# Kernel tuning notes

Measured on AMD Instinct MI355X. Metric: run time of the kernel, lower is better.

Reference implementation:

```python
import jax, jax.numpy as jnp
import numpy as np

B, S, D = 8, 1024, 512
H, DH, OUT = 8, 64, 512
EPS = 1e-6

def _ln(x, scale, bias):
    m = jnp.mean(x, -1, keepdims=True)
    v = jnp.mean(jnp.square(x - m), -1, keepdims=True)
    return (x - m) * jax.lax.rsqrt(v + EPS) * scale + bias

def _rel_shift(x):
    # TransformerXL relative shift: [B,H,Q,P] -> [B,H,Q,P]
    b, h, q, p = x.shape
    x = jnp.pad(x, ((0, 0), (0, 0), (0, 0), (1, 0)))
    x = x.reshape(b, h, p + 1, q)
    return x[:, :, 1:, :].reshape(b, h, q, p)

def _gate(x, y, wry, wrx, wzy, wzx, why, whx, bg):
    # GTrXL GRU-style gating
    r = jax.nn.sigmoid(y @ wry + x @ wrx)
    z = jax.nn.sigmoid(y @ wzy + x @ wzx - bg)
    h = jnp.tanh(y @ why + (r * x) @ whx)
    return (1 - z) * x + z * h

def setup_inputs() -> dict:
    key = jax.random.key(0)
    ks = jax.random.split(key, 40)
    w = lambda k, shp: (0.02 * jax.random.normal(k, shp, jnp.float32))
    inp = {
        'values_keys': jax.random.normal(ks[0], (B, S, D), jnp.float32),
        'queries': jax.random.normal(ks[1], (B, S, D), jnp.float32),
        'pos_embed': jax.random.normal(ks[2], (S, D), jnp.float32),
        'mask': jnp.tril(jnp.ones((S, S), bool))[None, None],
        'ln1_scale': jnp.ones((D,), jnp.float32), 'ln1_bias': jnp.zeros((D,), jnp.float32),
        'wq': w(ks[3], (D, H, DH)), 'bq': jnp.zeros((H, DH), jnp.float32),
        'wk': w(ks[4], (D, H, DH)), 'bk': jnp.zeros((H, DH), jnp.float32),
        'wv': w(ks[5], (D, H, DH)), 'bv': jnp.zeros((H, DH), jnp.float32),
        'wr': w(ks[6], (D, H, DH)),
        'u_bias': w(ks[7], (H, DH)), 'v_bias': w(ks[8], (H, DH)),
        'wo': w(ks[9], (H, DH, OUT)), 'bo': jnp.zeros((OUT,), jnp.float32),
        'ln2_scale': jnp.ones((OUT,), jnp.float32), 'ln2_bias': jnp.zeros((OUT,), jnp.float32),
        'w1': w(ks[10], (OUT, OUT)), 'b1': jnp.zeros((OUT,), jnp.float32),
        'w2': w(ks[11], (OUT, OUT)), 'b2': jnp.zeros((OUT,), jnp.float32),
    }
    for gi, base in ((1, 12), (2, 19)):
        for j, nm in enumerate(['wry', 'wrx', 'wzy', 'wzx', 'why', 'whx']):
            inp['g%d_%s' % (gi, nm)] = w(ks[base + j], (OUT, OUT))
        inp['g%d_bg' % gi] = 2.0 * jnp.ones((OUT,), jnp.float32)
    return inp

def reference(values_keys, queries, pos_embed, mask, ln1_scale, ln1_bias, wq, bq, wk, bk, wv, bv, wr, u_bias, v_bias, wo, bo, ln2_scale, ln2_bias, w1, b1, w2, b2, g1_wry, g1_wrx, g1_wzy, g1_wzx, g1_why, g1_whx, g1_bg, g2_wry, g2_wrx, g2_wzy, g2_wzx, g2_why, g2_whx, g2_bg):
    vk = _ln(values_keys, ln1_scale, ln1_bias)
    qn = _ln(queries, ln1_scale, ln1_bias)
    q = jnp.einsum('bsd,dhk->bshk', qn, wq) + bq
    k = jnp.einsum('bsd,dhk->bshk', vk, wk) + bk
    v = jnp.einsum('bsd,dhk->bshk', vk, wv) + bv
    r = jnp.einsum('pd,dhk->phk', pos_embed, wr)
    ac = jnp.einsum('bqhk,bshk->bhqs', q + u_bias, k)
    bd = _rel_shift(jnp.einsum('bqhk,phk->bhqp', q + v_bias, r))
    scores = (ac + bd) * jnp.float32(1.0 / np.sqrt(DH))
    scores = jnp.where(mask, scores, jnp.float32(-1e9))
    attn = jax.nn.softmax(scores, axis=-1)
    o = jnp.einsum('bhqs,bshk->bqhk', attn, v)
    attn_out = jnp.einsum('bqhk,hko->bqo', o, wo) + bo
    out_attention = _gate(queries, jax.nn.relu(attn_out), g1_wry, g1_wrx, g1_wzy, g1_wzx, g1_why, g1_whx, g1_bg)
    h = _ln(out_attention, ln2_scale, ln2_bias)
    h = jax.nn.gelu(h @ w1 + b1) @ w2 + b2
    return _gate(h, jax.nn.relu(out_attention), g2_wry, g2_wrx, g2_wzy, g2_wzx, g2_why, g2_whx, g2_bg)
```

## Files before the change

kernel.cpp:

```cpp
#include <hip/hip_runtime.h>
#include <hip/hip_bf16.h>
#include <math.h>

#define TPB 256
#define B_   8
#define S_   1024
#define D_   512
#define H_   8
#define DH_  64
#define MTOK (B_ * S_)
#define NEL  (MTOK * D_)
#define WMAT (D_ * D_)

typedef __attribute__((ext_vector_type(8))) short bf8;
typedef __attribute__((ext_vector_type(4))) float f4;

__device__ __forceinline__ float ld_any(const void* p, long i, bool bf) {
  if (bf) {
    unsigned u = (unsigned)((const unsigned short*)p)[i];
    union { unsigned u; float f; } c; c.u = u << 16;
    return c.f;
  }
  return ((const float*)p)[i];
}

__device__ __forceinline__ unsigned short f2bf(float f) {
  union { float f; unsigned u; } c; c.f = f;
  unsigned u = c.u;
  u += 0x7FFFu + ((u >> 16) & 1u);
  return (unsigned short)(u >> 16);
}

typedef const void __attribute__((address_space(1)))* gp_t;
typedef void __attribute__((address_space(3)))* lp_t;
__device__ __forceinline__ void gl16(const void* g, void* l) {
  __builtin_amdgcn_global_load_lds((gp_t)(uintptr_t)g,
                                   (lp_t)(unsigned)(uintptr_t)l, 16, 0, 0);
}

struct P19 { const void* p[19]; };
struct P14 { const void* p[14]; };

__device__ __forceinline__ void ln_row_wave(
    const void* src, unsigned short* dst, long row,
    const void* scale, const void* bias, bool bf_s, bool bf_p, int lane,
    float* __restrict__ qF, unsigned short* __restrict__ qB) {
  const long base = row * 512 + lane * 8;
  float x[8];
  if (bf_s) {
    bf8 v = *(const bf8*)((const unsigned short*)src + base);
#pragma unroll
    for (int j = 0; j < 8; j++) {
      union { unsigned u; float f; } c;
      c.u = ((unsigned)(unsigned short)v[j]) << 16;
      x[j] = c.f;
    }
  } else {
    f4 a = *(const f4*)((const float*)src + base);
    f4 b = *(const f4*)((const float*)src + base + 4);
#pragma unroll
    for (int j = 0; j < 4; j++) { x[j] = a[j]; x[4 + j] = b[j]; }
  }
  if (qF) {
    f4 a, b;
#pragma unroll
    for (int j = 0; j < 4; j++) { a[j] = x[j]; b[j] = x[4 + j]; }
    *(f4*)(qF + base) = a;
    *(f4*)(qF + base + 4) = b;
    union { bf8 v; unsigned short s[8]; } q;
#pragma unroll
    for (int j = 0; j < 8; j++) q.s[j] = f2bf(x[j]);
    *(bf8*)(qB + base) = q.v;
  }
  float s = 0.f;
#pragma unroll
  for (int j = 0; j < 8; j++) s += x[j];
#pragma unroll
  for (int o = 1; o < 64; o <<= 1) s += __shfl_xor(s, o, 64);
  const float m = s * (1.0f / 512.0f);
  float vs = 0.f;
#pragma unroll
  for (int j = 0; j < 8; j++) { float d = x[j] - m; vs += d * d; }
#pragma unroll
  for (int o = 1; o < 64; o <<= 1) vs += __shfl_xor(vs, o, 64);
  const float inv = rsqrtf(vs * (1.0f / 512.0f) + 1e-6f);
  float sc[8], bi[8];
  if (bf_p) {
    bf8 vs_ = *(const bf8*)((const unsigned short*)scale + lane * 8);
    bf8 vb  = *(const bf8*)((const unsigned short*)bias + lane * 8);
#pragma unroll
    for (int j = 0; j < 8; j++) {
      union { unsigned u; float f; } c1, c2;
      c1.u = ((unsigned)(unsigned short)vs_[j]) << 16;
      c2.u = ((unsigned)(unsigned short)vb[j]) << 16;
      sc[j] = c1.f; bi[j] = c2.f;
    }
  } else {
    f4 s0 = *(const f4*)((const float*)scale + lane * 8);
    f4 s1 = *(const f4*)((const float*)scale + lane * 8 + 4);
    f4 b0 = *(const f4*)((const float*)bias + lane * 8);
    f4 b1 = *(const f4*)((const float*)bias + lane * 8 + 4);
#pragma unroll
    for (int j = 0; j < 4; j++) { sc[j] = s0[j]; sc[4 + j] = s1[j];
                                  bi[j] = b0[j]; bi[4 + j] = b1[j]; }
  }
  union { bf8 v; unsigned short s8[8]; } o;
#pragma unroll
  for (int j = 0; j < 8; j++) o.s8[j] = f2bf((x[j] - m) * inv * sc[j] + bi[j]);
  *(bf8*)(dst + base) = o.v;
}

__global__ __launch_bounds__(TPB) void k_prep(
    const void* __restrict__ vk_src, const void* __restrict__ q_src,
    const void* __restrict__ pos_src, const void* __restrict__ sc_src,
    const void* __restrict__ bi_src, P19 pw, P14 pp,
    unsigned short* __restrict__ vk_b, unsigned short* __restrict__ qn_b,
    float* __restrict__ qF, unsigned short* __restrict__ qB,
    unsigned short* __restrict__ posB, float* __restrict__ Pb,
    unsigned short* __restrict__ Wt, const unsigned* __restrict__ flagp) {
  __shared__ float smem[64 * 65];
  const bool bf = (*flagp == 0x3F803F80u);
  const int bx = blockIdx.x, t = threadIdx.x;
  const int lane = t & 63, w = t >> 6;
  if (bx < 4096) {
    long row = (long)bx * 4 + w;
    if (row < MTOK) {
      ln_row_wave(vk_src, vk_b, row, sc_src, bi_src, bf, bf, lane,
                  nullptr, nullptr);
    } else {
      ln_row_wave(q_src, qn_b, row - MTOK, sc_src, bi_src, bf, bf, lane,
                  qF, qB);
    }
  } else if (bx < 4608) {
    long i0 = ((long)(bx - 4096) * TPB + t) * 4;
#pragma unroll
    for (int j = 0; j < 4; j++) posB[i0 + j] = f2bf(ld_any(pos_src, i0 + j, bf));
  } else if (bx < 4636) {
    int i = (bx - 4608) * TPB + t;
    Pb[i] = ld_any(pp.p[i >> 9], i & 511, bf);
  } else {
    int zz = bx - 4636;
    int z = zz >> 6, tile = zz & 63;
    int k0 = (tile >> 3) * 64, n0 = (tile & 7) * 64;
    const void* src = pw.p[z];
    unsigned short* dst = Wt + (size_t)z * WMAT;
#pragma unroll
    for (int i = 0; i < 16; i++) {
      int fl = i * TPB + t;
      int r = fl >> 6, c = fl & 63;
      smem[r * 65 + c] = ld_any(src, (long)(k0 + r) * 512 + n0 + c, bf);
    }
    __syncthreads();
#pragma unroll
    for (int i = 0; i < 16; i++) {
      int fl = i * TPB + t;
      int r = fl >> 6, c = fl & 63;
      dst[(size_t)(n0 + r) * 512 + k0 + c] = f2bf(smem[c * 65 + r]);
    }
  }
}

__global__ __launch_bounds__(TPB) void k_ln_bf(const void* __restrict__ src,
                                               unsigned short* __restrict__ dst,
                                               const float* __restrict__ scale,
                                               const float* __restrict__ bias) {
  const int lane = threadIdx.x & 63, w = threadIdx.x >> 6;
  ln_row_wave(src, dst, (long)blockIdx.x * 4 + w, scale, bias, false, false,
              lane, nullptr, nullptr);
}

__global__ __launch_bounds__(TPB) void k_frag(
    const unsigned short* __restrict__ kB, const unsigned short* __restrict__ vTB,
    const unsigned short* __restrict__ rB, unsigned short* __restrict__ KF,
    unsigned short* __restrict__ VF, unsigned short* __restrict__ RF) {
  int c = blockIdx.x * TPB + threadIdx.x;
  if (c < 524288) {
    int col = c & 15, quad = (c >> 4) & 3, ks = (c >> 6) & 1, h = (c >> 7) & 7;
    int pg = (c >> 10) & 63, b = c >> 16;
    bf8 v = *(const bf8*)&kB[(size_t)(b * 1024 + pg * 16 + col) * 512 +
                             h * 64 + ks * 32 + quad * 8];
    *(bf8*)&KF[(size_t)c * 8] = v;
  } else if (c < 1048576) {
    int d = c - 524288;
    int col = d & 15, quad = (d >> 4) & 3, nd = (d >> 6) & 3, ks = (d >> 8) & 1;
    int pt = (d >> 9) & 15, h = (d >> 13) & 7, b = d >> 16;
    bf8 v = *(const bf8*)&vTB[(size_t)((b * 8 + h) * 64 + nd * 16 + col) * 1024 +
                              pt * 64 + ks * 32 + quad * 8];
    *(bf8*)&VF[(size_t)d * 8] = v;
  } else {
    int d = c - 1048576;
    int col = d & 15, quad = (d >> 4) & 3, ks = (d >> 6) & 1, g = (d >> 7) & 63;
    int h = d >> 13;
    bf8 v = *(const bf8*)&rB[(size_t)(g * 16 + col) * 512 +
                             h * 64 + ks * 32 + quad * 8];
    *(bf8*)&RF[(size_t)d * 8] = v;
  }
}

template <int ACT, bool DUAL>
__device__ __forceinline__ void gemm_core(
    unsigned short* As, unsigned short* Bs,
    const unsigned short* __restrict__ A1, const unsigned short* __restrict__ W1,
    const unsigned short* __restrict__ A2, const unsigned short* __restrict__ W2,
    const float* __restrict__ bias, const float* __restrict__ xb,
    const float* __restrict__ zb, const float* __restrict__ aux1,
    const float* __restrict__ aux2,
    float* __restrict__ outF, unsigned short* __restrict__ outB,
    unsigned short* __restrict__ outB2,
    const unsigned* __restrict__ flagp, int bm, int bn) {
  const int tid = threadIdx.x;
  const int w = tid >> 6, lane = tid & 63;
  const int quad = lane >> 4, col = lane & 15;
  const int wm = w >> 1, wn = w & 1;
  const int lrow = lane >> 3;
  const int lkc  = (lane & 7) ^ lrow;
  const int sw_base = col & 7;

  f4 acc[4][4];
#pragma unroll
  for (int mi = 0; mi < 4; mi++)
#pragma unroll
    for (int ni = 0; ni < 4; ni++) acc[mi][ni] = (f4){0.f, 0.f, 0.f, 0.f};

  auto stage = [&](const unsigned short* Ap, const unsigned short* Wp, int k0) {
#pragma unroll
    for (int i = 0; i < 4; i++) {
      gl16(Ap + (size_t)(bm + w * 32 + i * 8 + lrow) * 512 + k0 + lkc * 8,
           (char*)As + w * 4096 + i * 1024);
      gl16(Wp + (size_t)(bn + w * 32 + i * 8 + lrow) * 512 + k0 + lkc * 8,
           (char*)Bs + w * 4096 + i * 1024);
    }
  };
  auto compute = [&]() {
#pragma unroll
    for (int kk = 0; kk < 2; ++kk) {
      const int swz = (kk * 4 + quad) ^ sw_base;
      bf8 af[4], bfg[4];
#pragma unroll
      for (int mi = 0; mi < 4; mi++)
        af[mi] = *(const bf8*)&As[((wm * 64 + mi * 16 + col) * 8 + swz) * 8];
#pragma unroll
      for (int ni = 0; ni < 4; ni++)
        bfg[ni] = *(const bf8*)&Bs[((wn * 64 + ni * 16 + col) * 8 + swz) * 8];
#pragma unroll
      for (int mi = 0; mi < 4; mi++)
#pragma unroll
        for (int ni = 0; ni < 4; ni++)
          acc[mi][ni] = __builtin_amdgcn_mfma_f32_16x16x32_bf16(af[mi], bfg[ni],
                                                                acc[mi][ni], 0, 0, 0);
    }
  };

  for (int k0 = 0; k0 < 512; k0 += 64) {
    __syncthreads();
    stage(A1, W1, k0);
    __syncthreads();
    compute();
  }
  if constexpr (DUAL) {
    for (int k0 = 0; k0 < 512; k0 += 64) {
      __syncthreads();
      stage(A2, W2, k0);
      __syncthreads();
      compute();
    }
  }

  bool bfout = false;
  if constexpr (ACT == 7) bfout = (*flagp == 0x3F803F80u);
#pragma unroll
  for (int mi = 0; mi < 4; mi++)
#pragma unroll
    for (int ni = 0; ni < 4; ni++) {
      const int n = bn + wn * 64 + ni * 16 + col;
      const float bn_v = bias ? bias[n] : 0.f;
      const int m0 = bm + wm * 64 + mi * 16 + quad * 4;
      if (ACT == 11 && n >= 512) {
        unsigned long long pk = 0;
#pragma unroll
        for (int r = 0; r < 4; r++) {
          float v = acc[mi][ni][r] + bn_v;
          pk |= (unsigned long long)f2bf(v) << (16 * r);
        }
        size_t dst = ((size_t)(m0 >> 10) * 512 + (n - 512)) * 1024 + (m0 & 1023);
        *(unsigned long long*)&outB2[dst] = pk;
      } else {
#pragma unroll
        for (int r = 0; r < 4; r++) {
          size_t idx = (size_t)(m0 + r) * 512 + n;
          float v = acc[mi][ni][r] + bn_v;
          if (ACT == 0) {
            if (outF) outF[idx] = v;
            if (outB) outB[idx] = f2bf(v);
          } else if (ACT == 1) {
            outB[idx] = f2bf(fmaxf(v, 0.f));
          } else if (ACT == 5) {
            float z = zb[idx], x = xb[idx];
            float g = (1.f - z) * x + z * tanhf(v);
            outF[idx] = g;
            outB[idx] = f2bf(fmaxf(g, 0.f));
          } else if (ACT == 6) {
            float t = 0.7978845608028654f * (v + 0.044715f * v * v * v);
            outB[idx] = f2bf(0.5f * v * (1.f + tanhf(t)));
          } else if (ACT == 7) {
            float z = zb[idx], x = xb[idx];
            float g = (1.f - z) * x + z * tanhf(v);
            if (bfout) outB[idx] = f2bf(g);
            else       outF[idx] = g;
          } else if (ACT == 8) {
            outB[idx]  = f2bf(v + aux1[n]);
            outB2[idx] = f2bf(v + aux2[n]);
          } else if (ACT == 10) {
            if (n < 512) {
              outB[idx] = f2bf(xb[idx] / (1.f + __expf(-v)));
            } else {
              size_t zi = (size_t)(m0 + r) * 512 + (n - 512);
              outF[zi] = 1.f / (1.f + __expf(-(v - aux1[n - 512])));
            }
          } else if (ACT == 11) {
            outB[idx] = f2bf(v);
          }
        }
      }
    }
}

template <int ACT, bool DUAL>
__global__ __launch_bounds__(TPB) void k_gemm(
    const unsigned short* __restrict__ A1, const unsigned short* __restrict__ W1,
    const unsigned short* __restrict__ A2, const unsigned short* __restrict__ W2,
    const float* __restrict__ bias, const float* __restrict__ xb,
    const float* __restrict__ zb, const float* __restrict__ aux1,
    const float* __restrict__ aux2,
    float* __restrict__ outF, unsigned short* __restrict__ outB,
    unsigned short* __restrict__ outB2,
    const unsigned* __restrict__ flagp) {
  __shared__ unsigned short As[128 * 64];
  __shared__ unsigned short Bs[128 * 64];
  gemm_core<ACT, DUAL>(As, Bs, A1, W1, A2, W2, bias, xb, zb, aux1, aux2,
                       outF, outB, outB2, flagp,
                       blockIdx.x * 128, blockIdx.y * 128);
}

__global__ __launch_bounds__(TPB) void k_proj(
    const unsigned short* __restrict__ qn_b, const unsigned short* __restrict__ vk_b,
    const unsigned short* __restrict__ pos_b, const unsigned short* __restrict__ Wt,
    const float* __restrict__ Pb,
    unsigned short* __restrict__ qu_b, unsigned short* __restrict__ qv_b,
    unsigned short* __restrict__ k_b, unsigned short* __restrict__ vT,
    unsigned short* __restrict__ r_b) {
  __shared__ unsigned short As[128 * 64];
  __shared__ unsigned short Bs[128 * 64];
  const int bx = blockIdx.x;
  if (bx < 256) {
    int bm = (bx & 63) * 128, bn = (bx >> 6) * 128;
    gemm_core<8, false>(As, Bs, qn_b, Wt, nullptr, nullptr, Pb + 1024, nullptr,
                        nullptr, Pb + 2560, Pb + 3072, nullptr, qu_b, qv_b,
                        nullptr, bm, bn);
  } else if (bx < 768) {
    int t = bx - 256;
    int bm = (t & 63) * 128, bn = (t >> 6) * 128;
    gemm_core<11, false>(As, Bs, vk_b, Wt + (size_t)1 * WMAT, nullptr, nullptr,
                         Pb + 1536, nullptr, nullptr, nullptr, nullptr, nullptr,
                         k_b, vT, nullptr, bm, bn);
  } else {
    int t = bx - 768;
    int bm = (t & 7) * 128, bn = (t >> 3) * 128;
    gemm_core<0, false>(As, Bs, pos_b, Wt + (size_t)3 * WMAT, nullptr, nullptr,
                        nullptr, nullptr, nullptr, nullptr, nullptr, nullptr,
                        r_b, nullptr, nullptr, bm, bn);
  }
}

#define AC_STR 68
#define BD_STR 68

__global__ __launch_bounds__(64, 2) void k_attn8(
    const unsigned short* __restrict__ quB, const unsigned short* __restrict__ qvB,
    const unsigned short* __restrict__ KF, const unsigned short* __restrict__ VF,
    const unsigned short* __restrict__ RF, unsigned short* __restrict__ oB) {
  __shared__ float acS[16 * AC_STR];
  __shared__ float bdS[16 * BD_STR];
  const int lane = threadIdx.x;
  const int quad = lane >> 4, col = lane & 15;
  const int bx = blockIdx.x;
  const int bh = (bx & 7) * 8 + ((bx >> 3) & 7);
  const int qt = 63 - (bx >> 6);
  const int b = bh >> 3, h = bh & 7, dbase = h * 64;
  const int q0 = qt << 4;
  const int np = (qt >> 2) + 1;

  bf8 aqu[2], aqv[2];
  {
    const unsigned short* p1 = quB + (size_t)(b * 1024 + q0 + col) * 512 + dbase + quad * 8;
    const unsigned short* p2 = qvB + (size_t)(b * 1024 + q0 + col) * 512 + dbase + quad * 8;
    aqu[0] = *(const bf8*)p1; aqu[1] = *(const bf8*)(p1 + 32);
    aqv[0] = *(const bf8*)p2; aqv[1] = *(const bf8*)(p2 + 32);
  }
  f4 accO[4];
#pragma unroll
  for (int nd = 0; nd < 4; nd++) accO[nd] = (f4){0.f, 0.f, 0.f, 0.f};
  float lsum = 0.f;

  bf8 kreg[2][4], rreg[2][5], vreg[2][4];

  auto loadKR = [&](int pt) {
    const int pg = pt * 4;
    const int g0 = 63 - qt + pt * 4;
#pragma unroll
    for (int ks = 0; ks < 2; ++ks) {
#pragma unroll
      for (int ni = 0; ni < 4; ++ni) {
        size_t kidx = ((((size_t)b * 64 + pg + ni) * 8 + h) * 2 + ks) * 64 + lane;
        kreg[ks][ni] = *(const bf8*)&KF[kidx * 8];
      }
#pragma unroll
      for (int nj = 0; nj < 5; ++nj) {
        int g = g0 + nj; if (g > 63) g = 63;
        size_t ridx = (((size_t)h * 64 + g) * 2 + ks) * 64 + lane;
        rreg[ks][nj] = *(const bf8*)&RF[ridx * 8];
      }
    }
  };
  auto loadV = [&](int pt) {
#pragma unroll
    for (int ks = 0; ks < 2; ++ks)
#pragma unroll
      for (int nd = 0; nd < 4; ++nd) {
        size_t vidx = (((((size_t)b * 8 + h) * 16 + pt) * 2 + ks) * 4 + nd) * 64 + lane;
        vreg[ks][nd] = *(const bf8*)&VF[vidx * 8];
      }
  };

  loadKR(0);
  loadV(0);
  __builtin_amdgcn_sched_barrier(0);

#pragma unroll 1
  for (int pt = 0; pt < np; ++pt) {
    const int p0 = pt << 6;

    f4 ac[4], bd[5];
#pragma unroll
    for (int ni = 0; ni < 4; ni++) ac[ni] = (f4){0.f, 0.f, 0.f, 0.f};
#pragma unroll
    for (int nj = 0; nj < 5; nj++) bd[nj] = (f4){0.f, 0.f, 0.f, 0.f};
#pragma unroll
    for (int ks = 0; ks < 2; ++ks) {
#pragma unroll
      for (int ni = 0; ni < 4; ++ni)
        ac[ni] = __builtin_amdgcn_mfma_f32_16x16x32_bf16(aqu[ks], kreg[ks][ni],
                                                         ac[ni], 0, 0, 0);
#pragma unroll
      for (int nj = 0; nj < 5; ++nj)
        bd[nj] = __builtin_amdgcn_mfma_f32_16x16x32_bf16(aqv[ks], rreg[ks][nj],
                                                         bd[nj], 0, 0, 0);
    }
    __builtin_amdgcn_sched_barrier(0);

    if (pt + 1 < np) loadKR(pt + 1);
    __builtin_amdgcn_sched_barrier(0);

#pragma unroll
    for (int ni = 0; ni < 4; ++ni)
#pragma unroll
      for (int r = 0; r < 4; ++r)
        acS[(quad * 4 + r) * AC_STR + ni * 16 + col] = ac[ni][r];
#pragma unroll
    for (int nj = 0; nj < 5; ++nj)
#pragma unroll
      for (int r = 0; r < 4; ++r) {
        int row = quad * 4 + r;
        int idx = nj * 16 + col + row - 15;
        if ((unsigned)idx < 64u) bdS[row * BD_STR + idx] = bd[nj][r];
      }
    __asm__ volatile("s_waitcnt lgkmcnt(0)" ::: "memory");

    bf8 apf[2];
    const int qg = q0 + col;
#pragma unroll
    for (int ks = 0; ks < 2; ++ks) {
      const int po = ks * 32 + quad * 8;
      f4 A0 = *(const f4*)&acS[col * AC_STR + po];
      f4 A1 = *(const f4*)&acS[col * AC_STR + po + 4];
      f4 B0 = *(const f4*)&bdS[col * BD_STR + po];
      f4 B1 = *(const f4*)&bdS[col * BD_STR + po + 4];
      const int pb = p0 + po;
      union { bf8 v; unsigned short s[8]; } ap;
#pragma unroll
      for (int jj = 0; jj < 4; ++jj) {
        float e0 = (pb + jj <= qg) ? __expf((A0[jj] + B0[jj]) * 0.125f) : 0.f;
        float e1 = (pb + 4 + jj <= qg) ? __expf((A1[jj] + B1[jj]) * 0.125f) : 0.f;
        lsum += e0 + e1;
        ap.s[jj] = f2bf(e0); ap.s[4 + jj] = f2bf(e1);
      }
      apf[ks] = ap.v;
    }

#pragma unroll
    for (int ks = 0; ks < 2; ++ks) {
#pragma unroll
      for (int nd = 0; nd < 4; ++nd)
        accO[nd] = __builtin_amdgcn_mfma_f32_16x16x32_bf16(apf[ks], vreg[ks][nd],
                                                           accO[nd], 0, 0, 0);
    }
    __builtin_amdgcn_sched_barrier(0);

    if (pt + 1 < np) loadV(pt + 1);
    __builtin_amdgcn_sched_barrier(0);
  }

  float ls = lsum;
  ls += __shfl_xor(ls, 16, 64);
  ls += __shfl_xor(ls, 32, 64);
  float lr[4];
#pragma unroll
  for (int r = 0; r < 4; ++r) lr[r] = __shfl(ls, quad * 4 + r, 64);
#pragma unroll
  for (int nd = 0; nd < 4; ++nd)
#pragma unroll
    for (int r = 0; r < 4; ++r) {
      float o = accO[nd][r] / lr[r];
      oB[(size_t)(b * 1024 + q0 + quad * 4 + r) * 512 + dbase + nd * 16 + col] = f2bf(o);
    }
}

extern "C" void kernel_launch(void* const* d_in, const int* in_sizes, int n_in,
                              void* d_out, int out_size, void* d_ws, size_t ws_size,
                              hipStream_t stream) {
  (void)in_sizes; (void)n_in; (void)out_size; (void)ws_size;
  const unsigned* flagp = (const unsigned*)d_in[4];
  char* ws = (char*)d_ws;
  const size_t MB = 1u << 20;
  auto SH = [&](int i) { return (unsigned short*)(ws + (size_t)i * 8 * MB); };

  unsigned short* vk_b = SH(0);
  unsigned short* qn_b = SH(1);
  unsigned short* qu_b = SH(2);
  unsigned short* qv_b = SH(3);
  unsigned short* k_b  = SH(4);
  unsigned short* qr_b = SH(5);
  unsigned short* vT   = SH(6);
  unsigned short* posr = SH(7);
  float* qF = (float*)(ws + 64 * MB);
  float* z1 = (float*)(ws + 80 * MB);
  float* oa = (float*)(ws + 96 * MB);
  unsigned short* Wt = (unsigned short*)(ws + 112 * MB);
  float* Pb = (float*)(ws + 122 * MB);

  unsigned short* KF = (unsigned short*)(ws + 80 * MB);
  unsigned short* RF = (unsigned short*)(ws + 88 * MB);
  unsigned short* VF = (unsigned short*)(ws + 96 * MB);

  unsigned short* pos_b = posr;
  unsigned short* r_b   = posr + 524288;
  unsigned short* o_b = qn_b;  unsigned short* y1 = vk_b;
  unsigned short* rx1 = qu_b;  unsigned short* y2 = qv_b;
  unsigned short* ln2h = k_b;  unsigned short* hg = qr_b;
  unsigned short* h_b = vT;    unsigned short* rx2 = posr;
  float* hF = qF;              float* z2 = z1;

  auto W = [&](int i) { return Wt + (size_t)i * WMAT; };
  dim3 bt(TPB);
  dim3 gG(MTOK / 128, 4);
  dim3 gG2(MTOK / 128, 8);

  P19 pw; const int wi[19] = {6, 8, 10, 12, 15, 19, 21,
                              23, 25, 24, 26, 27, 28, 30, 32, 31, 33, 34, 35};
  for (int i = 0; i < 19; i++) pw.p[i] = d_in[wi[i]];
  P14 pp; const int pi[14] = {4, 5, 7, 9, 11, 13, 14, 16, 17, 18, 20, 22, 29, 36};
  for (int i = 0; i < 14; i++) pp.p[i] = d_in[pi[i]];

  k_prep<<<dim3(5852), bt, 0, stream>>>(d_in[0], d_in[1], d_in[2], d_in[4],
                                        d_in[5], pw, pp, vk_b, qn_b, qF, qr_b,
                                        pos_b, Pb, Wt, flagp);

  k_proj<<<dim3(800), bt, 0, stream>>>(qn_b, vk_b, pos_b, Wt, Pb,
                                       qu_b, qv_b, k_b, vT, r_b);

  k_frag<<<dim3(4352), bt, 0, stream>>>(k_b, vT, r_b, KF, VF, RF);

  k_attn8<<<dim3(4096), dim3(64), 0, stream>>>(qu_b, qv_b, KF, VF, RF, o_b);

  k_gemm<1, false><<<gG, bt, 0, stream>>>(o_b, W(4), nullptr, nullptr,
                                          Pb + 3584, nullptr, nullptr, nullptr,
                                          nullptr, nullptr, y1, nullptr,
                                          nullptr);
  k_gemm<10, true><<<gG2, bt, 0, stream>>>(y1, W(7), qr_b, W(9), nullptr, qF,
                                           nullptr, Pb + 6144, nullptr, z1,
                                           rx1, nullptr, nullptr);
  k_gemm<5, true><<<gG, bt, 0, stream>>>(y1, W(11), rx1, W(12), nullptr, qF,
                                         z1, nullptr, nullptr, oa, y2, nullptr,
                                         nullptr);

  k_ln_bf<<<dim3(MTOK / 4), bt, 0, stream>>>(oa, ln2h, Pb + 4096, Pb + 4608);
  k_gemm<6, false><<<gG, bt, 0, stream>>>(ln2h, W(5), nullptr, nullptr,
                                          Pb + 5120, nullptr, nullptr, nullptr,
                                          nullptr, nullptr, hg, nullptr,
                                          nullptr);
  k_gemm<0, false><<<gG, bt, 0, stream>>>(hg, W(6), nullptr, nullptr,
                                          Pb + 5632, nullptr, nullptr, nullptr,
                                          nullptr, hF, h_b, nullptr,
                                          nullptr);

  k_gemm<10, true><<<gG2, bt, 0, stream>>>(y2, W(13), h_b, W(15), nullptr, hF,
                                           nullptr, Pb + 6656, nullptr, z2,
                                           rx2, nullptr, nullptr);
  k_gemm<7, true><<<gG, bt, 0, stream>>>(y2, W(17), rx2, W(18), nullptr, hF,
                                         z2, nullptr, nullptr, (float*)d_out,
                                         (unsigned short*)d_out, nullptr,
                                         flagp);
}
```

Before: 462.1 us.

## Double-buffer LDS tiles in GEMM core to overlap global loads with MFMA

Converts the shared GEMM core from a single LDS buffer with two barriers per k-step into a two-stage ping-pong pipeline. The next tile is loaded into the alternate buffer while the current one feeds the MFMAs, and the dual-GEMM case is folded into one unified 16-step loop. This aims to hide global-load latency behind compute. In exchange, LDS use per block doubles to 64KB, which may cut occupancy, and explicit waitcnt plus barrier pairs are added per step.

```diff
diff --git a/kernel.cpp b/kernel.cpp
--- a/kernel.cpp
+++ b/kernel.cpp
@@ -215,6 +215,7 @@
   const int lrow = lane >> 3;
   const int lkc  = (lane & 7) ^ lrow;
   const int sw_base = col & 7;
+  constexpr int NT = DUAL ? 16 : 8;
 
   f4 acc[4][4];
 #pragma unroll
@@ -222,26 +223,34 @@
 #pragma unroll
     for (int ni = 0; ni < 4; ni++) acc[mi][ni] = (f4){0.f, 0.f, 0.f, 0.f};
 
-  auto stage = [&](const unsigned short* Ap, const unsigned short* Wp, int k0) {
+  const unsigned short* A2p = DUAL ? A2 : A1;
+  const unsigned short* W2p = DUAL ? W2 : W1;
+
+  auto stage = [&](int buf, int t) {
+    const unsigned short* Ap = (t < 8) ? A1 : A2p;
+    const unsigned short* Wp = (t < 8) ? W1 : W2p;
+    const int k0 = (t & 7) * 64;
 #pragma unroll
     for (int i = 0; i < 4; i++) {
       gl16(Ap + (size_t)(bm + w * 32 + i * 8 + lrow) * 512 + k0 + lkc * 8,
-           (char*)As + w * 4096 + i * 1024);
+           (char*)As + buf * 16384 + w * 4096 + i * 1024);
       gl16(Wp + (size_t)(bn + w * 32 + i * 8 + lrow) * 512 + k0 + lkc * 8,
-           (char*)Bs + w * 4096 + i * 1024);
+           (char*)Bs + buf * 16384 + w * 4096 + i * 1024);
     }
   };
-  auto compute = [&]() {
+  auto compute = [&](int buf) {
+    const unsigned short* Ab = As + buf * 8192;
+    const unsigned short* Bb = Bs + buf * 8192;
 #pragma unroll
     for (int kk = 0; kk < 2; ++kk) {
       const int swz = (kk * 4 + quad) ^ sw_base;
       bf8 af[4], bfg[4];
 #pragma unroll
       for (int mi = 0; mi < 4; mi++)
-        af[mi] = *(const bf8*)&As[((wm * 64 + mi * 16 + col) * 8 + swz) * 8];
+        af[mi] = *(const bf8*)&Ab[((wm * 64 + mi * 16 + col) * 8 + swz) * 8];
 #pragma unroll
       for (int ni = 0; ni < 4; ni++)
-        bfg[ni] = *(const bf8*)&Bs[((wn * 64 + ni * 16 + col) * 8 + swz) * 8];
+        bfg[ni] = *(const bf8*)&Bb[((wn * 64 + ni * 16 + col) * 8 + swz) * 8];
 #pragma unroll
       for (int mi = 0; mi < 4; mi++)
 #pragma unroll
@@ -251,19 +260,19 @@
     }
   };
 
-  for (int k0 = 0; k0 < 512; k0 += 64) {
-    __syncthreads();
-    stage(A1, W1, k0);
-    __syncthreads();
-    compute();
-  }
-  if constexpr (DUAL) {
-    for (int k0 = 0; k0 < 512; k0 += 64) {
-      __syncthreads();
-      stage(A2, W2, k0);
-      __syncthreads();
-      compute();
-    }
+  stage(0, 0);
+  __asm__ volatile("s_waitcnt vmcnt(0)" ::: "memory");
+  __builtin_amdgcn_s_barrier();
+
+  for (int t = 0; t < NT; t += 2) {
+    stage(1, t + 1);
+    compute(0);
+    __asm__ volatile("s_waitcnt vmcnt(0) lgkmcnt(0)" ::: "memory");
+    __builtin_amdgcn_s_barrier();
+    if (t + 2 < NT) stage(0, t + 2);
+    compute(1);
+    __asm__ volatile("s_waitcnt vmcnt(0) lgkmcnt(0)" ::: "memory");
+    __builtin_amdgcn_s_barrier();
   }
 
   bool bfout = false;
@@ -300,8 +309,8 @@
             outF[idx] = g;
             outB[idx] = f2bf(fmaxf(g, 0.f));
           } else if (ACT == 6) {
-            float t = 0.7978845608028654f * (v + 0.044715f * v * v * v);
-            outB[idx] = f2bf(0.5f * v * (1.f + tanhf(t)));
+            float t2 = 0.7978845608028654f * (v + 0.044715f * v * v * v);
+            outB[idx] = f2bf(0.5f * v * (1.f + tanhf(t2)));
           } else if (ACT == 7) {
             float z = zb[idx], x = xb[idx];
             float g = (1.f - z) * x + z * tanhf(v);
@@ -335,8 +344,8 @@
     float* __restrict__ outF, unsigned short* __restrict__ outB,
     unsigned short* __restrict__ outB2,
     const unsigned* __restrict__ flagp) {
-  __shared__ unsigned short As[128 * 64];
-  __shared__ unsigned short Bs[128 * 64];
+  __shared__ unsigned short As[2 * 128 * 64];
+  __shared__ unsigned short Bs[2 * 128 * 64];
   gemm_core<ACT, DUAL>(As, Bs, A1, W1, A2, W2, bias, xb, zb, aux1, aux2,
                        outF, outB, outB2, flagp,
                        blockIdx.x * 128, blockIdx.y * 128);
@@ -349,8 +358,8 @@
     unsigned short* __restrict__ qu_b, unsigned short* __restrict__ qv_b,
     unsigned short* __restrict__ k_b, unsigned short* __restrict__ vT,
     unsigned short* __restrict__ r_b) {
-  __shared__ unsigned short As[128 * 64];
-  __shared__ unsigned short Bs[128 * 64];
+  __shared__ unsigned short As[2 * 128 * 64];
+  __shared__ unsigned short Bs[2 * 128 * 64];
   const int bx = blockIdx.x;
   if (bx < 256) {
     int bm = (bx & 63) * 128, bn = (bx >> 6) * 128;
```

Measured after the change: 441.6 us. 1.05x faster.
